# Optimization experiments

Hardware: AMD Instinct MI355X
Metric: run time of the kernel (lower is better)

## Reference

```python
import jax, jax.numpy as jnp
import numpy as np

B, N, C = 8, 4096, 512
NUM_HEADS = 8
HEAD_DIM = C // NUM_HEADS
POS_RES = 32  # only table with res <= max_resolution=32


def _interp_linear(pos, out_len):
    # F.interpolate(mode='linear', align_corners=False) along the length axis (axis 1)
    in_len = pos.shape[1]
    scale = in_len / out_len
    coords = (jnp.arange(out_len, dtype=jnp.float32) + 0.5) * scale - 0.5
    coords = jnp.clip(coords, 0.0, in_len - 1)
    i0 = jnp.floor(coords).astype(jnp.int32)
    i1 = jnp.minimum(i0 + 1, in_len - 1)
    w = (coords - i0.astype(jnp.float32))[None, :, None]
    return pos[:, i0, :] * (1.0 - w) + pos[:, i1, :] * w


def setup_inputs():
    key = jax.random.key(0)
    k = jax.random.split(key, 4)
    x = jax.random.normal(k[0], (B, N, C), jnp.float32)
    pos_32 = jax.random.normal(k[1], (1, POS_RES ** 3, C), jnp.float32)  # torch.randn init
    s = 1.0 / np.sqrt(C)
    w_qkv = jax.random.normal(k[2], (C, 3 * C), jnp.float32) * s
    b_qkv = jnp.zeros((3 * C,), jnp.float32)
    w_proj = jax.random.normal(k[3], (C, C), jnp.float32) * s
    b_proj = jnp.zeros((C,), jnp.float32)
    return {"x": x, "pos_32": pos_32, "w_qkv": w_qkv, "b_qkv": b_qkv,
            "w_proj": w_proj, "b_proj": b_proj, "resolution": 16}


def reference(x, pos_32, w_qkv, b_qkv, w_proj, b_proj, resolution):
    Bx, Nx, Cx = x.shape
    target_len = resolution ** 3  # 4096 -> nearest table pos_32 is interpolated down
    pos = pos_32 if pos_32.shape[1] == target_len else _interp_linear(pos_32, target_len)
    if pos.shape[1] == Nx:
        x = x + pos
    qkv = (x @ w_qkv + b_qkv).reshape(Bx, Nx, 3, NUM_HEADS, HEAD_DIM)
    q, k, v = qkv[:, :, 0], qkv[:, :, 1], qkv[:, :, 2]  # each [B, N, H, D]
    # Faithful to source: q,k,v are NOT permuted to [B,H,N,D], so q @ k.T
    # contracts head_dim per token, yielding [B, N, H, H] head-axis attention.
    attn = jnp.einsum('bnid,bnjd->bnij', q, k) / np.sqrt(HEAD_DIM)
    attn = jax.nn.softmax(attn, axis=-1)
    out = jnp.einsum('bnij,bnjd->bnid', attn, v)  # [B, N, H, D]
    # torch: .transpose(1, 2).reshape(B, N, C) -> flatten of [B, H, N, D]
    out = jnp.transpose(out, (0, 2, 1, 3)).reshape(Bx, Nx, Cx)
    return out @ w_proj + b_proj
```

## Files before the change

### kernel.cpp

```cpp
#include <hip/hip_runtime.h>
#include <hip/hip_bf16.h>

using bf16 = __hip_bfloat16;
typedef __attribute__((ext_vector_type(8))) short short8;
typedef __attribute__((ext_vector_type(4))) float f32x4;

#define AS1U(p) ((const __attribute__((address_space(1))) unsigned int*)(p))
#define AS3U(p) ((__attribute__((address_space(3))) unsigned int*)(p))

__device__ __forceinline__ float bflo(unsigned u) { return __uint_as_float(u << 16); }
__device__ __forceinline__ float bfhi(unsigned u) { return __uint_as_float(u & 0xffff0000u); }
__device__ __forceinline__ unsigned short f2bf(float f) {
    union { float f; unsigned u; } v{f};
    unsigned r = v.u + 0x7fffu + ((v.u >> 16) & 1u);
    return (unsigned short)(r >> 16);
}

__global__ __launch_bounds__(256) void kprep(const float* __restrict__ wq,
                                             const float* __restrict__ wp,
                                             const float* __restrict__ x,
                                             const float* __restrict__ pos,
                                             bf16* __restrict__ wqT,
                                             bf16* __restrict__ wpT,
                                             bf16* __restrict__ xp) {
    int bid = blockIdx.x;
    __shared__ float t[32][33];
    if (bid < 1024) {
        const float* in; bf16* out; int Cc, bx, by;
        if (bid < 768) { in = wq; out = wqT; Cc = 1536; bx = bid % 48; by = bid / 48; }
        else { int i = bid - 768; in = wp; out = wpT; Cc = 512; bx = i & 15; by = i >> 4; }
        const int R = 512;
        int tx = threadIdx.x & 31, ty = threadIdx.x >> 5;
        int c0 = bx * 32, r0 = by * 32;
#pragma unroll
        for (int i = 0; i < 4; ++i)
            t[ty + i * 8][tx] = in[(size_t)(r0 + ty + i * 8) * Cc + c0 + tx];
        __syncthreads();
#pragma unroll
        for (int i = 0; i < 4; ++i)
            out[(size_t)(c0 + ty + i * 8) * R + r0 + tx] = __float2bfloat16(t[tx][ty + i * 8]);
    } else {
        size_t idx8 = (size_t)(bid - 1024) * 256 + threadIdx.x;
        size_t e = idx8 * 8;
        int c = (int)(e & 511);
        int n = (int)((e >> 9) & 4095);
        const float* xs = x + e;
        const float* p3 = pos + (size_t)(n * 8 + 3) * 512 + c;
        const float* p4 = pos + (size_t)(n * 8 + 4) * 512 + c;
        unsigned r[4];
#pragma unroll
        for (int h = 0; h < 2; ++h) {
            float4 xv = *(const float4*)(xs + h * 4);
            float4 a = *(const float4*)(p3 + h * 4);
            float4 b = *(const float4*)(p4 + h * 4);
            float v0 = xv.x + 0.5f * (a.x + b.x);
            float v1 = xv.y + 0.5f * (a.y + b.y);
            float v2 = xv.z + 0.5f * (a.z + b.z);
            float v3 = xv.w + 0.5f * (a.w + b.w);
            r[h * 2]     = (unsigned)f2bf(v0) | ((unsigned)f2bf(v1) << 16);
            r[h * 2 + 1] = (unsigned)f2bf(v2) | ((unsigned)f2bf(v3) << 16);
        }
        *(uint4*)(xp + e) = *(uint4*)r;
    }
}


template <typename OutT>
__global__ __launch_bounds__(512, 2) void kgemm8(const bf16* __restrict__ A,
                                                 const bf16* __restrict__ Bt,
                                                 const float* __restrict__ bias,
                                                 OutT* __restrict__ C,
                                                 int M, int N, int K_) {
    constexpr int K = 512;
    __shared__ __align__(16) char smem[131072];
    const int tid = threadIdx.x;
    const int lane = tid & 63, wave = tid >> 6;
    const int wm = wave >> 2, wn = wave & 3;
    const int fr = lane & 15;
    const int g = lane >> 4;

    const int p_rd = (((fr & 1) << 2) | g) ^ ((fr >> 1) & 7);
    const int tbA = (wm * 64 + (fr >> 1)) * 128 + p_rd * 16;
    const int tbB = (wn * 32 + (fr >> 1)) * 128 + p_rd * 16;

    const int ntn = N >> 8;
    const int nwg = gridDim.x;
    const int bid = blockIdx.x;
    const int swz = (bid & 7) * (nwg >> 3) + (bid >> 3);
    const int bm = (swz / ntn) << 8;
    const int bn = (swz % ntn) << 8;

    const int q = (lane & 7) ^ (lane >> 3);
    const int srow = wave * 32 + 2 * (lane >> 3) + ((q >> 2) & 1);
    const int scol = (q & 3) * 8;
    const bf16* sA[2]; const bf16* sB[2];
#pragma unroll
    for (int g2 = 0; g2 < 2; ++g2) {
        sA[g2] = A  + (size_t)(bm + srow + g2 * 16) * K + scol;
        sB[g2] = Bt + (size_t)(bn + srow + g2 * 16) * K + scol;
    }
    const int dA0 = wave * 2048, dA1 = wave * 2048 + 1024;

    f32x4 acc[8][4];
#pragma unroll
    for (int i = 0; i < 8; ++i)
#pragma unroll
        for (int j = 0; j < 4; ++j) acc[i][j] = f32x4{0.f, 0.f, 0.f, 0.f};

    auto stageA = [&](int kt, int slot) {
        char* d = smem + slot * 32768;
        __builtin_amdgcn_global_load_lds(AS1U(sA[0] + kt * 32), AS3U(d + dA0), 16, 0, 0);
        __builtin_amdgcn_global_load_lds(AS1U(sA[1] + kt * 32), AS3U(d + dA1), 16, 0, 0);
    };
    auto stageB = [&](int kt, int slot) {
        char* d = smem + slot * 32768 + 16384;
        __builtin_amdgcn_global_load_lds(AS1U(sB[0] + kt * 32), AS3U(d + dA0), 16, 0, 0);
        __builtin_amdgcn_global_load_lds(AS1U(sB[1] + kt * 32), AS3U(d + dA1), 16, 0, 0);
    };

    stageA(0, 0); stageB(0, 0);
    stageA(1, 1); stageB(1, 1);
    stageA(2, 2); stageB(2, 2);
    asm volatile("s_waitcnt vmcnt(8)" ::: "memory");
    __builtin_amdgcn_s_barrier();

#pragma unroll
    for (int t = 0; t < 16; ++t) {
        const int rd = t & 3, wrs = (t + 3) & 3;
        const char* pa = smem + rd * 32768;
        const char* pb = pa + 16384;
        if (t < 13) { stageA(t + 3, wrs); stageB(t + 3, wrs); }
        short8 af[8], bfr[4];
#pragma unroll
        for (int mi = 0; mi < 8; ++mi) af[mi] = *(const short8*)(pa + tbA + mi * 1024);
#pragma unroll
        for (int nj = 0; nj < 4; ++nj) bfr[nj] = *(const short8*)(pb + tbB + nj * 1024);
#pragma unroll
        for (int mi = 0; mi < 8; ++mi)
#pragma unroll
            for (int nj = 0; nj < 4; ++nj)
                acc[mi][nj] = __builtin_amdgcn_mfma_f32_16x16x32_bf16(af[mi], bfr[nj], acc[mi][nj], 0, 0, 0);
        asm volatile("s_waitcnt lgkmcnt(0)" ::: "memory");
        if (t <= 12)      asm volatile("s_waitcnt vmcnt(8)" ::: "memory");
        else if (t == 13) asm volatile("s_waitcnt vmcnt(4)" ::: "memory");
        else if (t == 14) asm volatile("s_waitcnt vmcnt(0)" ::: "memory");
        __builtin_amdgcn_sched_barrier(0);
        __builtin_amdgcn_s_barrier();
    }

#pragma unroll
    for (int mi = 0; mi < 8; ++mi) {
#pragma unroll
        for (int nj = 0; nj < 4; ++nj) {
            int col = bn + wn * 64 + nj * 16 + fr;
            int row0 = bm + wm * 128 + mi * 16 + (lane >> 4) * 4;
            float bv = bias[col];
#pragma unroll
            for (int rr = 0; rr < 4; ++rr) {
                float val = acc[mi][nj][rr] + bv;
                if constexpr (sizeof(OutT) == 2)
                    C[(size_t)(row0 + rr) * N + col] = (OutT)__float2bfloat16(val);
                else
                    C[(size_t)(row0 + rr) * N + col] = (OutT)val;
            }
        }
    }
}

__global__ __launch_bounds__(256) void kattn(const bf16* __restrict__ qkv,
                                             bf16* __restrict__ oscr) {
    int T = blockIdx.x * 256 + threadIdx.x;
    int token = T >> 3, head = T & 7;
    int b = token >> 12, n = token & 4095;
    const bf16* row = qkv + (size_t)token * 1536;

    uint4 qp[8];
#pragma unroll
    for (int c = 0; c < 8; ++c) qp[c] = *(const uint4*)(row + head * 64 + c * 8);

    float s[8];
#pragma unroll
    for (int j = 0; j < 8; ++j) {
        float acc = 0.f;
#pragma unroll
        for (int c = 0; c < 8; ++c) {
            uint4 kp = *(const uint4*)(row + 512 + j * 64 + c * 8);
            const unsigned* ku = &kp.x; const unsigned* qu = &qp[c].x;
#pragma unroll
            for (int w = 0; w < 4; ++w) {
                acc = fmaf(bflo(qu[w]), bflo(ku[w]), acc);
                acc = fmaf(bfhi(qu[w]), bfhi(ku[w]), acc);
            }
        }
        s[j] = acc * 0.125f;
    }
    float mx = s[0];
#pragma unroll
    for (int j = 1; j < 8; ++j) mx = fmaxf(mx, s[j]);
    float sum = 0.f;
#pragma unroll
    for (int j = 0; j < 8; ++j) { s[j] = __expf(s[j] - mx); sum += s[j]; }
    float inv = 1.f / sum;
#pragma unroll
    for (int j = 0; j < 8; ++j) s[j] *= inv;

    float o[64];
#pragma unroll
    for (int d = 0; d < 64; ++d) o[d] = 0.f;
#pragma unroll
    for (int j = 0; j < 8; ++j) {
        float pj = s[j];
#pragma unroll
        for (int c = 0; c < 8; ++c) {
            uint4 vp = *(const uint4*)(row + 1024 + j * 64 + c * 8);
            const unsigned* vu = &vp.x;
#pragma unroll
            for (int w = 0; w < 4; ++w) {
                o[c * 8 + w * 2]     = fmaf(pj, bflo(vu[w]), o[c * 8 + w * 2]);
                o[c * 8 + w * 2 + 1] = fmaf(pj, bfhi(vu[w]), o[c * 8 + w * 2 + 1]);
            }
        }
    }
    size_t orow = (size_t)b * 4096 + head * 512 + (n >> 3);
    bf16* op = oscr + orow * 512 + (n & 7) * 64;
#pragma unroll
    for (int c = 0; c < 8; ++c) {
        unsigned rr[4];
#pragma unroll
        for (int w = 0; w < 4; ++w)
            rr[w] = (unsigned)f2bf(o[c * 8 + w * 2]) | ((unsigned)f2bf(o[c * 8 + w * 2 + 1]) << 16);
        *(uint4*)(op + c * 8) = *(uint4*)rr;
    }
}

extern "C" void kernel_launch(void* const* d_in, const int* in_sizes, int n_in,
                              void* d_out, int out_size, void* d_ws, size_t ws_size,
                              hipStream_t stream) {
    const float* x      = (const float*)d_in[0];
    const float* pos32  = (const float*)d_in[1];
    const float* w_qkv  = (const float*)d_in[2];
    const float* b_qkv  = (const float*)d_in[3];
    const float* w_proj = (const float*)d_in[4];
    const float* b_proj = (const float*)d_in[5];

    char* ws = (char*)d_ws;
    bf16* xp   = (bf16*)(ws);
    bf16* qkv  = (bf16*)(ws + 33554432);
    bf16* wqT  = (bf16*)(ws + 134217728);
    bf16* wpT  = (bf16*)(ws + 135790592);
    bf16* ascr = xp;

    kprep<<<9216, 256, 0, stream>>>(w_qkv, w_proj, x, pos32, wqT, wpT, xp);
    kgemm8<bf16><<<768, 512, 0, stream>>>(xp, wqT, b_qkv, qkv, 32768, 1536, 512);
    kattn<<<1024, 256, 0, stream>>>(qkv, ascr);
    kgemm8<float><<<256, 512, 0, stream>>>(ascr, wpT, b_proj, (float*)d_out, 32768, 512, 512);
}
```

Baseline: 141.2 us.

## Process two K-tiles per barrier in GEMM main loop with prefetch-two pipeline

Restructures the 4-slot LDS pipeline of the bf16 MFMA GEMM so each loop iteration consumes two K-tiles and issues loads for the next two. This halves the number of workgroup barriers and waitcnt stalls per GEMM. In exchange the prefetch distance shrinks from three tiles ahead to two, and each barrier drains all outstanding global loads with vmcnt(0), which may expose more memory latency. Register pressure also rises from holding two sets of fragments.

```diff
diff --git a/kernel.cpp b/kernel.cpp
--- a/kernel.cpp
+++ b/kernel.cpp
@@ -120,32 +120,45 @@
 
     stageA(0, 0); stageB(0, 0);
     stageA(1, 1); stageB(1, 1);
-    stageA(2, 2); stageB(2, 2);
-    asm volatile("s_waitcnt vmcnt(8)" ::: "memory");
+    asm volatile("s_waitcnt vmcnt(0)" ::: "memory");
     __builtin_amdgcn_s_barrier();
 
 #pragma unroll
-    for (int t = 0; t < 16; ++t) {
-        const int rd = t & 3, wrs = (t + 3) & 3;
-        const char* pa = smem + rd * 32768;
-        const char* pb = pa + 16384;
-        if (t < 13) { stageA(t + 3, wrs); stageB(t + 3, wrs); }
-        short8 af[8], bfr[4];
-#pragma unroll
-        for (int mi = 0; mi < 8; ++mi) af[mi] = *(const short8*)(pa + tbA + mi * 1024);
-#pragma unroll
-        for (int nj = 0; nj < 4; ++nj) bfr[nj] = *(const short8*)(pb + tbB + nj * 1024);
+    for (int ta = 0; ta < 8; ++ta) {
+        const int t0 = 2 * ta, t1 = t0 + 1;
+        const char* pa0 = smem + (t0 & 3) * 32768;
+        const char* pb0 = pa0 + 16384;
+        const char* pa1 = smem + (t1 & 3) * 32768;
+        const char* pb1 = pa1 + 16384;
+        if (ta < 7) {
+            stageA(t0 + 2, (t0 + 2) & 3); stageB(t0 + 2, (t0 + 2) & 3);
+            stageA(t1 + 2, (t1 + 2) & 3); stageB(t1 + 2, (t1 + 2) & 3);
+        }
+        short8 af0[8], bf0[4], af1[8], bf1[4];
+#pragma unroll
+        for (int mi = 0; mi < 8; ++mi) af0[mi] = *(const short8*)(pa0 + tbA + mi * 1024);
+#pragma unroll
+        for (int nj = 0; nj < 4; ++nj) bf0[nj] = *(const short8*)(pb0 + tbB + nj * 1024);
 #pragma unroll
         for (int mi = 0; mi < 8; ++mi)
 #pragma unroll
             for (int nj = 0; nj < 4; ++nj)
-                acc[mi][nj] = __builtin_amdgcn_mfma_f32_16x16x32_bf16(af[mi], bfr[nj], acc[mi][nj], 0, 0, 0);
-        asm volatile("s_waitcnt lgkmcnt(0)" ::: "memory");
-        if (t <= 12)      asm volatile("s_waitcnt vmcnt(8)" ::: "memory");
-        else if (t == 13) asm volatile("s_waitcnt vmcnt(4)" ::: "memory");
-        else if (t == 14) asm volatile("s_waitcnt vmcnt(0)" ::: "memory");
-        __builtin_amdgcn_sched_barrier(0);
-        __builtin_amdgcn_s_barrier();
+                acc[mi][nj] = __builtin_amdgcn_mfma_f32_16x16x32_bf16(af0[mi], bf0[nj], acc[mi][nj], 0, 0, 0);
+#pragma unroll
+        for (int mi = 0; mi < 8; ++mi) af1[mi] = *(const short8*)(pa1 + tbA + mi * 1024);
+#pragma unroll
+        for (int nj = 0; nj < 4; ++nj) bf1[nj] = *(const short8*)(pb1 + tbB + nj * 1024);
+#pragma unroll
+        for (int mi = 0; mi < 8; ++mi)
+#pragma unroll
+            for (int nj = 0; nj < 4; ++nj)
+                acc[mi][nj] = __builtin_amdgcn_mfma_f32_16x16x32_bf16(af1[mi], bf1[nj], acc[mi][nj], 0, 0, 0);
+        if (ta < 7) {
+            asm volatile("s_waitcnt lgkmcnt(0)" ::: "memory");
+            asm volatile("s_waitcnt vmcnt(0)" ::: "memory");
+            __builtin_amdgcn_sched_barrier(0);
+            __builtin_amdgcn_s_barrier();
+        }
     }
 
 #pragma unroll
```

Measured after the change: 156.4 us. +10.7%, slower.
